# Optimization experiments

Hardware: AMD Instinct MI355X
Metric: run time of the kernel (lower is better)

Reference implementation:

```python
import jax, jax.numpy as jnp
import numpy as np

D_MODEL = 512
D_STATE = 64
LN_EPS = 1e-3  # Keras LayerNormalization default epsilon


def setup_inputs() -> dict:
    key = jax.random.key(0)
    ks = jax.random.split(key, 12)
    B, S, D, N = 8, 4096, D_MODEL, D_STATE

    def glorot(k, shape):
        fan_in, fan_out = shape[0], shape[1]
        lim = np.sqrt(6.0 / (fan_in + fan_out)).astype(np.float32)
        return jax.random.uniform(k, shape, jnp.float32, -lim, lim)

    return {
        "x": jax.random.normal(ks[0], (B, S, D), jnp.float32),
        "ln_gamma": jnp.ones((D,), jnp.float32),
        "ln_beta": jnp.zeros((D,), jnp.float32),
        "W_in": glorot(ks[1], (D, D)),
        "b_in": jnp.zeros((D,), jnp.float32),
        "W_xs": glorot(ks[2], (D, N)),
        "W_B": glorot(ks[3], (D, N)),
        "b_B": jnp.zeros((N,), jnp.float32),
        "W_C": glorot(ks[4], (D, N)),
        "b_C": jnp.zeros((N,), jnp.float32),
        "A_log": jax.random.uniform(ks[5], (N,), jnp.float32, -4.0, -1.0),
        "D_skip": jnp.ones((D,), jnp.float32),
        "W_so": glorot(ks[6], (N, D)),
        "W_out": glorot(ks[7], (D, D)),
        "b_out": jnp.zeros((D,), jnp.float32),
    }


def reference(x, ln_gamma, ln_beta, W_in, b_in, W_xs, W_B, b_B, W_C, b_C,
              A_log, D_skip, W_so, W_out, b_out):
    residual = x
    # LayerNorm over last axis (Keras default eps=1e-3)
    mu = jnp.mean(x, axis=-1, keepdims=True)
    var = jnp.mean(jnp.square(x - mu), axis=-1, keepdims=True)
    xn = (x - mu) * jax.lax.rsqrt(var + LN_EPS) * ln_gamma + ln_beta
    # input projection (this projected x is what feeds the D skip too)
    xp = xn @ W_in + b_in                      # [B, S, D]
    Bmat = xp @ W_B + b_B                      # [B, S, N] selective B(x)
    Cmat = xp @ W_C + b_C                      # [B, S, N] selective C(x)
    xs = xp @ W_xs                             # [B, S, N]
    A_bar = jnp.exp(-jnp.exp(A_log))           # [N], stable decay in (0,1)
    Bx = Bmat * xs                             # per-step drive B_t * x_state_t

    # sequential scan: h_t = A_bar * h_{t-1} + Bx_t
    def step(h, bx):
        h = A_bar * h + bx
        return h, h

    h0 = jnp.zeros((x.shape[0], A_log.shape[0]), x.dtype)
    _, hs = jax.lax.scan(step, h0, jnp.swapaxes(Bx, 0, 1))  # hs: [S, B, N]
    hs = jnp.swapaxes(hs, 0, 1)                             # [B, S, N]

    y = jnp.einsum('bsn,nd->bsd', Cmat * hs, W_so) + D_skip * xp
    y = y @ W_out + b_out
    # dropout is identity at inference (training=None)
    return y + residual
```

## Files before the change

### kernel.cpp

```cpp
#include <hip/hip_runtime.h>
#include <cstdint>
#include <cstddef>


typedef unsigned short bf16_t;
typedef __attribute__((ext_vector_type(8))) short bh8;
typedef __attribute__((ext_vector_type(4))) float f4;

#define M_ROWS 32768
#define SCAN_L 16
#define SCAN_C 256

__device__ __forceinline__ unsigned short f2bf(float f) {
  union { float f; unsigned int u; } c; c.f = f;
  unsigned int u = c.u;
  return (unsigned short)((u + 0x7FFFu + ((u >> 16) & 1u)) >> 16);
}

__device__ __forceinline__ uint2 pack4bf(f4 a) {
  uint2 r;
  r.x = (unsigned)f2bf(a[0]) | ((unsigned)f2bf(a[1]) << 16);
  r.y = (unsigned)f2bf(a[2]) | ((unsigned)f2bf(a[3]) << 16);
  return r;
}

__device__ __forceinline__ void async_cp16(void* lds, const void* g) {
  __builtin_amdgcn_global_load_lds((const __attribute__((address_space(1))) void*)g,
                                   (__attribute__((address_space(3))) void*)lds, 16, 0, 0);
}

__global__ __launch_bounds__(256) void prep_all(
    const float* __restrict__ W_in, const float* __restrict__ W_out,
    const float* __restrict__ W_so, const float* __restrict__ W_xs,
    const float* __restrict__ W_B,  const float* __restrict__ W_C,
    const float* __restrict__ b_in, const float* __restrict__ D_skip,
    const float* __restrict__ A_log,
    bf16_t* __restrict__ Wout_t, bf16_t* __restrict__ Wdout_t,
    bf16_t* __restrict__ Win_b, bf16_t* __restrict__ Wso_b,
    bf16_t* __restrict__ Wcat_t, bf16_t* __restrict__ Wproj,
    float* __restrict__ Abar, float* __restrict__ Apow) {
  int i = blockIdx.x * 256 + threadIdx.x;
  if (i < 262144) { int k = i >> 9, n = i & 511;
    Wout_t[(size_t)n * 512 + k] = f2bf(W_out[k * 512 + n]); return; }
  i -= 262144;
  if (i < 262144) { int k = i >> 9, n = i & 511;
    Wdout_t[(size_t)n * 512 + k] = f2bf(D_skip[k] * W_out[k * 512 + n]); return; }
  i -= 262144;
  if (i < 262144) { Win_b[i] = f2bf(W_in[i]); return; }
  i -= 262144;
  if (i < 65536) { int r = i >> 9, j = i & 511;
    Win_b[(size_t)(512 + r) * 512 + j] = (r == 0) ? f2bf(b_in[j]) : (bf16_t)0; return; }
  i -= 65536;
  if (i < 65536) { int k = i >> 9, j = i & 511;
    Wso_b[i] = (k < 64) ? f2bf(W_so[k * 512 + j]) : (bf16_t)0; return; }
  i -= 65536;
  if (i < 131072) { int k = i >> 8, n = i & 255;
    float v = 0.f;
    if (n < 128) { int g = n >> 5, w = n & 31;
      v = (w < 16) ? W_xs[k * 64 + g * 16 + w] : W_B[k * 64 + g * 16 + (w - 16)];
    } else if (n < 192) v = W_C[k * 64 + n - 128];
    Wcat_t[(size_t)n * 512 + k] = f2bf(v); return; }
  i -= 131072;
  if (i < 32768) { int r = i >> 9, d = i & 511;
    Wproj[(size_t)(192 + r) * 512 + d] = 0; return; }
  i -= 32768;
  if (i < 64) {
    float a = __expf(A_log[i]);
    Abar[i] = __expf(-a);
    Apow[i] = __expf(-a * (float)SCAN_L);
  }
}

__global__ __launch_bounds__(256, 4) void prep2_fused(
    const bf16_t* __restrict__ Win_b, const bf16_t* __restrict__ Wcat_t,
    const bf16_t* __restrict__ Wso_b, const bf16_t* __restrict__ Wout_t,
    const bf16_t* __restrict__ Wdout_t,
    const float* __restrict__ b_B, const float* __restrict__ b_C,
    bf16_t* __restrict__ Wproj, bf16_t* __restrict__ Wcat2,
    float* __restrict__ biasp, float* __restrict__ biasW2,
    const float* __restrict__ x, const float* __restrict__ gamma,
    const float* __restrict__ beta, bf16_t* __restrict__ xn) {
  __shared__ __align__(16) bf16_t As[128 * 64];
  __shared__ __align__(16) bf16_t Bs[128 * 64];
  const int tid = threadIdx.x;

  if (blockIdx.x >= 34) {
    const int row = (int)(blockIdx.x - 34) * 4 + (tid >> 6);
    const int lane = tid & 63;
    const float* xr = x + (size_t)row * 512 + lane * 8;
    float4 v0 = *(const float4*)xr;
    float4 v1 = *(const float4*)(xr + 4);
    float s  = v0.x + v0.y + v0.z + v0.w + v1.x + v1.y + v1.z + v1.w;
    float sq = v0.x*v0.x + v0.y*v0.y + v0.z*v0.z + v0.w*v0.w
             + v1.x*v1.x + v1.y*v1.y + v1.z*v1.z + v1.w*v1.w;
    #pragma unroll
    for (int off = 32; off > 0; off >>= 1) {
      s  += __shfl_xor(s, off, 64);
      sq += __shfl_xor(sq, off, 64);
    }
    const float mu  = s * (1.0f / 512.0f);
    const float var = sq * (1.0f / 512.0f) - mu * mu;
    const float rs  = rsqrtf(var + 1e-3f);
    float4 g0 = *(const float4*)(gamma + lane * 8);
    float4 g1 = *(const float4*)(gamma + lane * 8 + 4);
    float4 b0 = *(const float4*)(beta + lane * 8);
    float4 b1 = *(const float4*)(beta + lane * 8 + 4);
    bh8 ov;
    ov[0] = (short)f2bf((v0.x - mu) * rs * g0.x + b0.x);
    ov[1] = (short)f2bf((v0.y - mu) * rs * g0.y + b0.y);
    ov[2] = (short)f2bf((v0.z - mu) * rs * g0.z + b0.z);
    ov[3] = (short)f2bf((v0.w - mu) * rs * g0.w + b0.w);
    ov[4] = (short)f2bf((v1.x - mu) * rs * g1.x + b1.x);
    ov[5] = (short)f2bf((v1.y - mu) * rs * g1.y + b1.y);
    ov[6] = (short)f2bf((v1.z - mu) * rs * g1.z + b1.z);
    ov[7] = (short)f2bf((v1.w - mu) * rs * g1.w + b1.w);
    *(bh8*)(xn + (size_t)row * 512 + lane * 8) = ov;
    return;
  }

  const int bx = blockIdx.x;
  const int wave = tid >> 6, lane = tid & 63;
  const int quad = lane >> 4, l16 = lane & 15;
  const int wm = (wave >> 1) * 64, wn = (wave & 1) * 64;
  int role, mb, nb;
  if (bx < 10)      { role = 0; mb = bx >> 1; nb = bx & 1; }
  else if (bx < 14) { role = 1; mb = 0; nb = bx - 10; }
  else { role = 2; int t = bx - 14; mb = t >> 2; nb = t & 3; }
  const bf16_t* Ap = (role == 1) ? Wso_b : Win_b;
  const bf16_t* Bp = (role == 0) ? Wcat_t : (role == 1) ? Wout_t : Wdout_t;

  f4 acc[4][4];
  #pragma unroll
  for (int i = 0; i < 4; ++i)
    #pragma unroll
    for (int j = 0; j < 4; ++j) acc[i][j] = (f4){0.f, 0.f, 0.f, 0.f};

  for (int kt = 0; kt < 8; ++kt) {
    const int k0 = kt << 6;
    __syncthreads();
    #pragma unroll
    for (int i = 0; i < 4; ++i) {
      const int base = (wave * 4 + i) * 64;
      const int cid = base + lane;
      const int row = cid >> 3;
      const int g = (cid & 7) ^ (row & 7);
      async_cp16((char*)As + base * 16,
                 Ap + (size_t)(mb * 128 + row) * 512 + k0 + g * 8);
    }
    #pragma unroll
    for (int i = 0; i < 4; ++i) {
      const int base = (wave * 4 + i) * 64;
      const int cid = base + lane;
      const int row = cid >> 3;
      const int g = (cid & 7) ^ (row & 7);
      async_cp16((char*)Bs + base * 16,
                 Bp + (size_t)(nb * 128 + row) * 512 + k0 + g * 8);
    }
    __syncthreads();
    #pragma unroll
    for (int ks = 0; ks < 2; ++ks) {
      const int gb = ks * 4 + quad;
      bh8 af[4], bfv[4];
      #pragma unroll
      for (int im = 0; im < 4; ++im) {
        const int row = wm + im * 16 + l16;
        af[im] = *(const bh8*)((const char*)As + row * 128 + ((gb ^ (row & 7)) * 16));
      }
      #pragma unroll
      for (int in_ = 0; in_ < 4; ++in_) {
        const int row = wn + in_ * 16 + l16;
        bfv[in_] = *(const bh8*)((const char*)Bs + row * 128 + ((gb ^ (row & 7)) * 16));
      }
      #pragma unroll
      for (int im = 0; im < 4; ++im)
        #pragma unroll
        for (int in_ = 0; in_ < 4; ++in_)
          acc[im][in_] = __builtin_amdgcn_mfma_f32_16x16x32_bf16(af[im], bfv[in_],
                                                                 acc[im][in_], 0, 0, 0);
    }
  }

  #pragma unroll
  for (int im = 0; im < 4; ++im) {
    #pragma unroll
    for (int in_ = 0; in_ < 4; ++in_) {
      const int row0 = mb * 128 + wm + im * 16 + quad * 4;
      const int col = nb * 128 + wn + in_ * 16 + l16;
      if (role == 0) {
        if (col < 192) {
          if (row0 < 512) {
            *(uint2*)(Wproj + (size_t)col * 512 + row0) = pack4bf(acc[im][in_]);
          } else if (row0 == 512) {
            float v = acc[im][in_][0];
            if (col < 128) { int w = col & 31;
              if (w >= 16) v += b_B[(col >> 5) * 16 + (w - 16)];
            } else v += b_C[col - 128];
            biasp[col] = v;
          }
        }
      } else if (role == 1) {
        if (row0 < 64)
          *(uint2*)(Wcat2 + (size_t)col * 576 + row0) = pack4bf(acc[im][in_]);
      } else {
        if (row0 < 512) {
          *(uint2*)(Wcat2 + (size_t)col * 576 + 64 + row0) = pack4bf(acc[im][in_]);
        } else if (row0 == 512) {
          biasW2[col] = acc[im][in_][0];
        }
      }
    }
  }
}

__global__ __launch_bounds__(256, 4) void gemm_proj(
    const bf16_t* __restrict__ A0, const bf16_t* __restrict__ Wt,
    float* __restrict__ outf, const float* __restrict__ bias1,
    const float* __restrict__ Abar, float* __restrict__ carryT) {
  __shared__ __align__(16) char smem[32768];
  bf16_t* As = (bf16_t*)smem;
  bf16_t* Bs = (bf16_t*)(smem + 16384);
  const int tid = threadIdx.x;
  const int wave = tid >> 6, lane = tid & 63;
  const int quad = lane >> 4, l16 = lane & 15;
  const int wm = (wave >> 1) * 64, wn = (wave & 1) * 64;
  const int mb = blockIdx.x, nb = blockIdx.y;
  const int K = 512;

  f4 acc[4][4];
  #pragma unroll
  for (int i = 0; i < 4; ++i)
    #pragma unroll
    for (int j = 0; j < 4; ++j) acc[i][j] = (f4){0.f, 0.f, 0.f, 0.f};

  for (int kt = 0; kt < 8; ++kt) {
    const int k0 = kt << 6;
    __syncthreads();
    #pragma unroll
    for (int i = 0; i < 4; ++i) {
      const int base = (wave * 4 + i) * 64;
      const int cid = base + lane;
      const int row = cid >> 3;
      const int g = (cid & 7) ^ (row & 7);
      async_cp16((char*)As + base * 16,
                 A0 + (size_t)(mb * 128 + row) * K + k0 + g * 8);
    }
    #pragma unroll
    for (int i = 0; i < 4; ++i) {
      const int base = (wave * 4 + i) * 64;
      const int cid = base + lane;
      const int row = cid >> 3;
      const int g = (cid & 7) ^ (row & 7);
      async_cp16((char*)Bs + base * 16,
                 Wt + (size_t)(nb * 128 + row) * K + k0 + g * 8);
    }
    __syncthreads();

    #pragma unroll
    for (int ks = 0; ks < 2; ++ks) {
      const int gb = ks * 4 + quad;
      bh8 af[4], bfv[4];
      #pragma unroll
      for (int im = 0; im < 4; ++im) {
        const int row = wm + im * 16 + l16;
        af[im] = *(const bh8*)((const char*)As + row * 128 + ((gb ^ (row & 7)) * 16));
      }
      #pragma unroll
      for (int in_ = 0; in_ < 4; ++in_) {
        const int row = wn + in_ * 16 + l16;
        bfv[in_] = *(const bh8*)((const char*)Bs + row * 128 + ((gb ^ (row & 7)) * 16));
      }
      #pragma unroll
      for (int im = 0; im < 4; ++im)
        #pragma unroll
        for (int in_ = 0; in_ < 4; ++in_)
          acc[im][in_] = __builtin_amdgcn_mfma_f32_16x16x32_bf16(af[im], bfv[in_],
                                                                 acc[im][in_], 0, 0, 0);
    }
  }

  __syncthreads();
  float* lt = (float*)smem;

  if (nb == 0) {
    float* wb = lt + wave * 2048;
    #pragma unroll
    for (int im = 0; im < 4; ++im)
      #pragma unroll
      for (int pp = 0; pp < 2; ++pp)
        #pragma unroll
        for (int r = 0; r < 4; ++r) {
          const int c0 = wn + (2 * pp) * 16 + l16;
          const float vx = acc[im][2 * pp][r]     + bias1[c0];
          const float vb = acc[im][2 * pp + 1][r] + bias1[c0 + 16];
          wb[(im * 16 + quad * 4 + r) * 32 + pp * 16 + l16] = vx * vb;
        }
    const int rsub = lane >> 3, cg8 = lane & 7;
    #pragma unroll
    for (int rr = 0; rr < 8; ++rr) {
      const int rl = rr * 8 + rsub;
      f4 v = *(f4*)(wb + rl * 32 + cg8 * 4);
      const size_t row = (size_t)(mb * 128 + wm + rl);
      *(f4*)(outf + row * 64 + (wn >> 1) + cg8 * 4) = v;
    }
    {
      const int bb = mb >> 5;
      const int cbase = (mb & 31) * 8 + (wm >> 4);
      const int ch = lane & 31;
      const int n = (wn >> 1) + ch;
      const float A = Abar[n];
      #pragma unroll
      for (int t = 0; t < 2; ++t) {
        const int cl = (lane >> 5) + 2 * t;
        float hv = 0.f;
        #pragma unroll
        for (int i = 0; i < SCAN_L; ++i)
          hv = fmaf(A, hv, wb[(cl * SCAN_L + i) * 32 + ch]);
        carryT[(size_t)(cbase + cl) * 512 + bb * 64 + n] = hv;
      }
    }
  } else if (wn == 0) {
    float* wb = lt + (wave >> 1) * 4096;
    #pragma unroll
    for (int im = 0; im < 4; ++im)
      #pragma unroll
      for (int in_ = 0; in_ < 4; ++in_)
        #pragma unroll
        for (int r = 0; r < 4; ++r) {
          const int c = in_ * 16 + l16;
          wb[(im * 16 + quad * 4 + r) * 64 + c] = acc[im][in_][r] + bias1[128 + c];
        }
    #pragma unroll
    for (int rr = 0; rr < 16; ++rr) {
      const int rl = rr * 4 + quad;
      f4 v = *(f4*)(wb + rl * 64 + l16 * 4);
      const size_t row = (size_t)(mb * 128 + wm + rl);
      *(f4*)(outf + ((size_t)M_ROWS + row) * 64 + l16 * 4) = v;
    }
  }
}

__global__ __launch_bounds__(256, 4) void gemm_out(
    const float* __restrict__ projP, const float* __restrict__ Abar,
    const float* __restrict__ Apow, const float* __restrict__ carryT,
    const bf16_t* __restrict__ xn, const bf16_t* __restrict__ Wt,
    float* __restrict__ outf,
    const float* __restrict__ bias0, const float* __restrict__ bias1,
    const float* __restrict__ resid) {
  __shared__ __align__(16) bf16_t As[64 * 64];
  __shared__ __align__(16) bf16_t Bs[128 * 64];
  const int tid = threadIdx.x;
  const int wave = tid >> 6, lane = tid & 63;
  const int quad = lane >> 4, l16 = lane & 15;
  const int wm = (wave >> 1) * 32, wn = (wave & 1) * 64;
  const int mb = blockIdx.x, nb = blockIdx.y;
  const int K = 576;

  {
    const int n = lane;
    const int cl = wave;
    const int bb = mb >> 6;
    const int c0 = (mb & 63) * 4 + cl;
    const float A = Abar[n];
    const float Ap = Apow[n];
    const float Ap4 = (Ap * Ap) * (Ap * Ap);
    const float* cr = carryT + bb * 64 + n;
    float h0 = 0.f, h1 = 0.f, h2 = 0.f, h3 = 0.f;
    int j = 0;
    for (; j + 4 <= c0; j += 4) {
      h0 = fmaf(Ap4, h0, cr[(size_t)j * 512]);
      h1 = fmaf(Ap4, h1, cr[(size_t)(j + 1) * 512]);
      h2 = fmaf(Ap4, h2, cr[(size_t)(j + 2) * 512]);
      h3 = fmaf(Ap4, h3, cr[(size_t)(j + 3) * 512]);
    }
    float h = fmaf(Ap, fmaf(Ap, fmaf(Ap, h0, h1), h2), h3);
    for (; j < c0; ++j) h = fmaf(Ap, h, cr[(size_t)j * 512]);
    const size_t row0 = (size_t)mb * 64 + cl * 16;
    const float* pBx = projP + row0 * 64;
    const float* pC  = projP + ((size_t)M_ROWS + row0) * 64;
    char* asb = (char*)As;
    const int g = n >> 3, boff = (n & 7) * 2;
    #pragma unroll
    for (int i = 0; i < SCAN_L; ++i) {
      h = fmaf(A, h, pBx[i * 64 + n]);
      const int row = cl * 16 + i;
      *(bf16_t*)(asb + row * 128 + ((g ^ (row & 7)) * 16) + boff) =
          f2bf(pC[i * 64 + n] * h);
    }
  }

  f4 acc[2][4];
  #pragma unroll
  for (int i = 0; i < 2; ++i)
    #pragma unroll
    for (int j = 0; j < 4; ++j) acc[i][j] = (f4){0.f, 0.f, 0.f, 0.f};

  for (int kt = 0; kt < 9; ++kt) {
    const int k0 = kt << 6;
    __syncthreads();
    if (kt > 0) {
      #pragma unroll
      for (int i = 0; i < 2; ++i) {
        const int base = (wave * 2 + i) * 64;
        const int cid = base + lane;
        const int row = cid >> 3;
        const int g = (cid & 7) ^ (row & 7);
        async_cp16((char*)As + base * 16,
                   xn + (size_t)(mb * 64 + row) * 512 + (k0 - 64) + g * 8);
      }
    }
    #pragma unroll
    for (int i = 0; i < 4; ++i) {
      const int base = (wave * 4 + i) * 64;
      const int cid = base + lane;
      const int row = cid >> 3;
      const int g = (cid & 7) ^ (row & 7);
      async_cp16((char*)Bs + base * 16,
                 Wt + (size_t)(nb * 128 + row) * K + k0 + g * 8);
    }
    __syncthreads();

    #pragma unroll
    for (int ks = 0; ks < 2; ++ks) {
      const int gb = ks * 4 + quad;
      bh8 af[2], bfv[4];
      #pragma unroll
      for (int im = 0; im < 2; ++im) {
        const int row = wm + im * 16 + l16;
        af[im] = *(const bh8*)((const char*)As + row * 128 + ((gb ^ (row & 7)) * 16));
      }
      #pragma unroll
      for (int in_ = 0; in_ < 4; ++in_) {
        const int row = wn + in_ * 16 + l16;
        bfv[in_] = *(const bh8*)((const char*)Bs + row * 128 + ((gb ^ (row & 7)) * 16));
      }
      #pragma unroll
      for (int im = 0; im < 2; ++im)
        #pragma unroll
        for (int in_ = 0; in_ < 4; ++in_)
          acc[im][in_] = __builtin_amdgcn_mfma_f32_16x16x32_bf16(af[im], bfv[in_],
                                                                 acc[im][in_], 0, 0, 0);
    }
  }

  #pragma unroll
  for (int im = 0; im < 2; ++im) {
    #pragma unroll
    for (int in_ = 0; in_ < 4; ++in_) {
      const int col = nb * 128 + wn + in_ * 16 + l16;
      const float bsum = bias0[col] + bias1[col];
      #pragma unroll
      for (int r = 0; r < 4; ++r) {
        const int row = mb * 64 + wm + im * 16 + quad * 4 + r;
        const size_t idx = (size_t)row * 512 + col;
        outf[idx] = acc[im][in_][r] + bsum + resid[idx];
      }
    }
  }
}

extern "C" void kernel_launch(void* const* d_in, const int* in_sizes, int n_in,
                              void* d_out, int out_size, void* d_ws, size_t ws_size,
                              hipStream_t stream) {
  const float* x      = (const float*)d_in[0];
  const float* ln_g   = (const float*)d_in[1];
  const float* ln_b   = (const float*)d_in[2];
  const float* W_in   = (const float*)d_in[3];
  const float* b_in   = (const float*)d_in[4];
  const float* W_xs   = (const float*)d_in[5];
  const float* W_B    = (const float*)d_in[6];
  const float* b_B    = (const float*)d_in[7];
  const float* W_C    = (const float*)d_in[8];
  const float* b_C    = (const float*)d_in[9];
  const float* A_log  = (const float*)d_in[10];
  const float* D_skip = (const float*)d_in[11];
  const float* W_so   = (const float*)d_in[12];
  const float* W_out  = (const float*)d_in[13];
  const float* b_out  = (const float*)d_in[14];
  float* out = (float*)d_out;

  char* w = (char*)d_ws;
  auto carve = [&](size_t bytes) {
    char* p = w; w += (bytes + 255) & ~(size_t)255; return p;
  };
  bf16_t* xn     = (bf16_t*)carve((size_t)M_ROWS * 512 * 2);
  float*  projP  = (float*)carve((size_t)2 * M_ROWS * 64 * 4);
  float*  carryT = (float*)carve((size_t)SCAN_C * 512 * 4);
  bf16_t* Wproj  = (bf16_t*)carve((size_t)256 * 512 * 2);
  bf16_t* Wcat2  = (bf16_t*)carve((size_t)512 * 576 * 2);
  bf16_t* Win_b  = (bf16_t*)carve((size_t)640 * 512 * 2);
  bf16_t* Wso_b  = (bf16_t*)carve((size_t)128 * 512 * 2);
  bf16_t* Wout_t = (bf16_t*)carve((size_t)512 * 512 * 2);
  bf16_t* Wdout_t= (bf16_t*)carve((size_t)512 * 512 * 2);
  bf16_t* Wcat_t = (bf16_t*)carve((size_t)256 * 512 * 2);
  float*  biasp  = (float*)carve(192 * 4);
  float*  biasW2 = (float*)carve(512 * 4);
  float*  Abar   = (float*)carve(256);
  float*  Apow   = (float*)carve(256);

  prep_all<<<4227, 256, 0, stream>>>(W_in, W_out, W_so, W_xs, W_B, W_C, b_in,
                                     D_skip, A_log, Wout_t, Wdout_t, Win_b,
                                     Wso_b, Wcat_t, Wproj, Abar, Apow);
  prep2_fused<<<34 + 8192, 256, 0, stream>>>(Win_b, Wcat_t, Wso_b, Wout_t,
                                             Wdout_t, b_B, b_C, Wproj, Wcat2,
                                             biasp, biasW2, x, ln_g, ln_b, xn);
  gemm_proj<<<dim3(256, 2), 256, 0, stream>>>(xn, Wproj, projP, biasp,
                                              Abar, carryT);
  gemm_out<<<dim3(512, 4), 256, 0, stream>>>(projP, Abar, Apow, carryT,
                                             xn, Wcat2, out,
                                             b_out, biasW2, x);
}
```

Baseline: 219.1 us.

## Precompute chunk carry prefixes in a separate scan kernel, prefetch weights early

Adds a small scan_prefix kernel that computes the exclusive prefix of chunk carries once per batch and state. gemm_out then reads its starting state directly instead of every wave redoing an O(chunks) serial recurrence over strided global loads. gemm_out also issues the first weight tile's async copies before the scan section, drops one barrier, and uses nontemporal load/store for the residual and output. The trade is an extra launch of a tiny, poorly parallel kernel (8 blocks of 64 threads serially walking 256 chunks) plus a small workspace buffer.

```diff
diff --git a/kernel.cpp b/kernel.cpp
--- a/kernel.cpp
+++ b/kernel.cpp
@@ -339,9 +339,29 @@
   }
 }
 
+__global__ __launch_bounds__(64) void scan_prefix(
+    const float* __restrict__ carryT, const float* __restrict__ Apow,
+    float* __restrict__ prefixT) {
+  const int bb = blockIdx.x, n = threadIdx.x;
+  const float Ap = Apow[n];
+  const float* cr = carryT + bb * 64 + n;
+  float* pf = prefixT + bb * 64 + n;
+  float h = 0.f;
+  for (int c = 0; c < SCAN_C; c += 16) {
+    float v[16];
+    #pragma unroll
+    for (int i = 0; i < 16; ++i) v[i] = cr[(size_t)(c + i) * 512];
+    #pragma unroll
+    for (int i = 0; i < 16; ++i) {
+      pf[(size_t)(c + i) * 512] = h;
+      h = fmaf(Ap, h, v[i]);
+    }
+  }
+}
+
 __global__ __launch_bounds__(256, 4) void gemm_out(
     const float* __restrict__ projP, const float* __restrict__ Abar,
-    const float* __restrict__ Apow, const float* __restrict__ carryT,
+    const float* __restrict__ prefixT,
     const bf16_t* __restrict__ xn, const bf16_t* __restrict__ Wt,
     float* __restrict__ outf,
     const float* __restrict__ bias0, const float* __restrict__ bias1,
@@ -355,25 +375,23 @@
   const int mb = blockIdx.x, nb = blockIdx.y;
   const int K = 576;
 
+  #pragma unroll
+  for (int i = 0; i < 4; ++i) {
+    const int base = (wave * 4 + i) * 64;
+    const int cid = base + lane;
+    const int row = cid >> 3;
+    const int g = (cid & 7) ^ (row & 7);
+    async_cp16((char*)Bs + base * 16,
+               Wt + (size_t)(nb * 128 + row) * K + g * 8);
+  }
+
   {
     const int n = lane;
     const int cl = wave;
     const int bb = mb >> 6;
     const int c0 = (mb & 63) * 4 + cl;
     const float A = Abar[n];
-    const float Ap = Apow[n];
-    const float Ap4 = (Ap * Ap) * (Ap * Ap);
-    const float* cr = carryT + bb * 64 + n;
-    float h0 = 0.f, h1 = 0.f, h2 = 0.f, h3 = 0.f;
-    int j = 0;
-    for (; j + 4 <= c0; j += 4) {
-      h0 = fmaf(Ap4, h0, cr[(size_t)j * 512]);
-      h1 = fmaf(Ap4, h1, cr[(size_t)(j + 1) * 512]);
-      h2 = fmaf(Ap4, h2, cr[(size_t)(j + 2) * 512]);
-      h3 = fmaf(Ap4, h3, cr[(size_t)(j + 3) * 512]);
-    }
-    float h = fmaf(Ap, fmaf(Ap, fmaf(Ap, h0, h1), h2), h3);
-    for (; j < c0; ++j) h = fmaf(Ap, h, cr[(size_t)j * 512]);
+    float h = prefixT[(size_t)c0 * 512 + bb * 64 + n];
     const size_t row0 = (size_t)mb * 64 + cl * 16;
     const float* pBx = projP + row0 * 64;
     const float* pC  = projP + ((size_t)M_ROWS + row0) * 64;
@@ -396,8 +414,8 @@
 
   for (int kt = 0; kt < 9; ++kt) {
     const int k0 = kt << 6;
-    __syncthreads();
     if (kt > 0) {
+      __syncthreads();
       #pragma unroll
       for (int i = 0; i < 2; ++i) {
         const int base = (wave * 2 + i) * 64;
@@ -407,15 +425,15 @@
         async_cp16((char*)As + base * 16,
                    xn + (size_t)(mb * 64 + row) * 512 + (k0 - 64) + g * 8);
       }
-    }
-    #pragma unroll
-    for (int i = 0; i < 4; ++i) {
-      const int base = (wave * 4 + i) * 64;
-      const int cid = base + lane;
-      const int row = cid >> 3;
-      const int g = (cid & 7) ^ (row & 7);
-      async_cp16((char*)Bs + base * 16,
-                 Wt + (size_t)(nb * 128 + row) * K + k0 + g * 8);
+      #pragma unroll
+      for (int i = 0; i < 4; ++i) {
+        const int base = (wave * 4 + i) * 64;
+        const int cid = base + lane;
+        const int row = cid >> 3;
+        const int g = (cid & 7) ^ (row & 7);
+        async_cp16((char*)Bs + base * 16,
+                   Wt + (size_t)(nb * 128 + row) * K + k0 + g * 8);
+      }
     }
     __syncthreads();
 
@@ -452,7 +470,8 @@
       for (int r = 0; r < 4; ++r) {
         const int row = mb * 64 + wm + im * 16 + quad * 4 + r;
         const size_t idx = (size_t)row * 512 + col;
-        outf[idx] = acc[im][in_][r] + bsum + resid[idx];
+        const float rv = __builtin_nontemporal_load(resid + idx);
+        __builtin_nontemporal_store(acc[im][in_][r] + bsum + rv, outf + idx);
       }
     }
   }
@@ -485,6 +504,7 @@
   bf16_t* xn     = (bf16_t*)carve((size_t)M_ROWS * 512 * 2);
   float*  projP  = (float*)carve((size_t)2 * M_ROWS * 64 * 4);
   float*  carryT = (float*)carve((size_t)SCAN_C * 512 * 4);
+  float*  prefixT= (float*)carve((size_t)SCAN_C * 512 * 4);
   bf16_t* Wproj  = (bf16_t*)carve((size_t)256 * 512 * 2);
   bf16_t* Wcat2  = (bf16_t*)carve((size_t)512 * 576 * 2);
   bf16_t* Win_b  = (bf16_t*)carve((size_t)640 * 512 * 2);
@@ -505,7 +525,8 @@
                                              biasp, biasW2, x, ln_g, ln_b, xn);
   gemm_proj<<<dim3(256, 2), 256, 0, stream>>>(xn, Wproj, projP, biasp,
                                               Abar, carryT);
-  gemm_out<<<dim3(512, 4), 256, 0, stream>>>(projP, Abar, Apow, carryT,
+  scan_prefix<<<8, 64, 0, stream>>>(carryT, Apow, prefixT);
+  gemm_out<<<dim3(512, 4), 256, 0, stream>>>(projP, Abar, prefixT,
                                              xn, Wcat2, out,
                                              b_out, biasW2, x);
 }
```

After: 231.7 us. +5.8%, slower.
